# Kernel optimization log

Hardware: AMD Instinct MI355X
Metric: run time of the kernel (lower is better)

## Reference

```python
import jax, jax.numpy as jnp
import numpy as np

B, T, D, R = 4, 2048, 1024, 64

def setup_inputs() -> dict:
    key = jax.random.key(0)
    ks = jax.random.split(key, 13)
    x = jax.random.normal(ks[0], (B, T, D), jnp.float32)
    # Linear weights stored torch-style [out, in]; applied as x @ W.T
    WQ = jax.random.normal(ks[1], (D, D), jnp.float32) * 0.02
    WK = jax.random.normal(ks[2], (D, D), jnp.float32) * 0.02
    WO = jax.random.normal(ks[3], (D, D), jnp.float32) * 0.02
    Winv = jnp.eye(D, dtype=jnp.float32) + 0.01 * jax.random.normal(ks[4], (D, D), jnp.float32)
    U_b = jax.random.normal(ks[5], (D, R), jnp.float32) * 0.02
    V_b = jax.random.normal(ks[6], (D, R), jnp.float32) * 0.02
    W_b = jax.random.normal(ks[7], (D, R), jnp.float32) * 0.02
    bias_b = jnp.zeros((D,), jnp.float32)
    U_t = jax.random.normal(ks[8], (D, R), jnp.float32) * 0.02
    V_t = jax.random.normal(ks[9], (D, R), jnp.float32) * 0.02
    W_t = jax.random.normal(ks[10], (D, R), jnp.float32) * 0.02
    X_t = jax.random.normal(ks[11], (D, R), jnp.float32) * 0.02
    bias_t = jnp.zeros((D,), jnp.float32)
    alpha_bi = jnp.float32(0.5)
    alpha_tri = jnp.float32(0.5)
    return {"x": x, "WQ": WQ, "WK": WK, "WO": WO, "Winv": Winv,
            "U_b": U_b, "V_b": V_b, "W_b": W_b, "bias_b": bias_b,
            "U_t": U_t, "V_t": V_t, "W_t": W_t, "X_t": X_t, "bias_t": bias_t,
            "alpha_bi": alpha_bi, "alpha_tri": alpha_tri}


def reference(x, WQ, WK, WO, Winv, U_b, V_b, W_b, bias_b,
              U_t, V_t, W_t, X_t, bias_t, alpha_bi, alpha_tri):
    # Faithful forward. The original materializes [B,T,T,D] pairwise tensors,
    # masks causally, sums over j and divides by n_valid. Because the (i,j)
    # score factorizes as f(i)*g(j) in rank space, sum_{j<=i} == f(i)*cumsum(g)_i,
    # so we use causal cumulative sums -- identical math, O(B*T*D*R) memory.
    Tlen = x.shape[1]
    Q = x @ WQ.T                       # [B,T,D]
    K = x @ WK.T
    invQ = Q @ Winv.T
    invK = K @ Winv.T
    counts = jnp.arange(1, Tlen + 1, dtype=x.dtype)[None, :, None]  # [1,T,1]
    z = jnp.cumsum(x, axis=1) / counts  # causal global mean, [B,T,D]
    # bilinear forward: sum_{j<=i} ((Q_i V_b) * (K_j W_b)) U_b^T + bias_b
    fwd_r = (Q @ V_b) * jnp.cumsum(K @ W_b, axis=1)          # [B,T,R]
    # bilinear inverse: sum_{j<=i} ((invK_j V_b) * (invQ_i W_b)) U_b^T + bias_b
    inv_r = jnp.cumsum(invK @ V_b, axis=1) * (invQ @ W_b)    # [B,T,R]
    # trilinear: sum_{j<=i} ((Q_i V_t)*(K_j W_t)*(Z_i X_t)) U_t^T + bias_t
    tri_r = (Q @ V_t) * jnp.cumsum(K @ W_t, axis=1) * (z @ X_t)  # [B,T,R]
    sum_fwd = fwd_r @ U_b.T + counts * bias_b                # [B,T,D]
    sum_inv = inv_r @ U_b.T + counts * bias_b
    sum_tri = tri_r @ U_t.T + counts * bias_t
    out = (sum_fwd + alpha_bi * sum_inv + alpha_tri * sum_tri) / counts
    return out @ WO.T
```

## Files before the change

kernel.cpp:

```cpp
#include <hip/hip_runtime.h>

#define T_LEN 2048
#define BT_DIM 8192

typedef __attribute__((ext_vector_type(8))) short s16x8;
typedef __attribute__((ext_vector_type(4))) float f32x4;

typedef __attribute__((address_space(1))) void gvoid_t;
typedef __attribute__((address_space(3))) void svoid_t;

__device__ __forceinline__ unsigned short f2bf(float f) {
  unsigned int u = __builtin_bit_cast(unsigned int, f);
  u += 0x7fffu + ((u >> 16) & 1u);
  return (unsigned short)(u >> 16);
}
__device__ __forceinline__ float bf2f(unsigned short u) {
  unsigned int v = (unsigned int)u << 16;
  return __builtin_bit_cast(float, v);
}
__device__ __forceinline__ void gload16(const void* g, void* l) {
  __builtin_amdgcn_global_load_lds((gvoid_t*)g, (svoid_t*)l, 16, 0, 0);
}

template<int EPI>
__device__ __forceinline__ void gemm_body(
    const unsigned short* __restrict__ A, const unsigned short* __restrict__ B,
    void* __restrict__ Cv, int lda, int ldb, int ldc, int K, int m0, int n0,
    const float* __restrict__ obias, float* __restrict__ sums, int ygrp,
    int rlo, int rhi)
{
  __shared__ unsigned short As[2 * 128 * 64];
  __shared__ unsigned short Bs[2 * 128 * 64];
  const int tid  = threadIdx.x;
  const int wave = tid >> 6;
  const int lane = tid & 63;
  const int wr = wave >> 1, wc = wave & 1;
  const int trow = tid >> 3;
  const int tcol = (tid & 7) << 3;

  const unsigned short* Ap = A + (size_t)(m0 + trow) * lda + tcol;
  const unsigned short* Bp = B + (size_t)(n0 + trow) * ldb + tcol;

  f32x4 acc[4][4] = {};

  auto stage = [&](int buf, int kt) {
    char* ab = (char*)As + buf * 16384 + wave * 1024;
    char* bb = (char*)Bs + buf * 16384 + wave * 1024;
#pragma unroll
    for (int it = 0; it < 4; ++it) {
      gload16(Ap + (size_t)it * 32 * lda + kt, ab + it * 4096);
      gload16(Bp + (size_t)it * 32 * ldb + kt, bb + it * 4096);
    }
  };

  stage(0, 0);
  __syncthreads();
  int cur = 0;
  for (int kt = 64; kt <= K; kt += 64) {
    if (kt < K) stage(cur ^ 1, kt);
#pragma unroll
    for (int ks = 0; ks < 2; ++ks) {
      const int kk = (ks << 5) + ((lane >> 4) << 3);
      const int ra = (wr << 6) + (lane & 15);
      const int rb = (wc << 6) + (lane & 15);
      s16x8 af[4], bfr[4];
#pragma unroll
      for (int i = 0; i < 4; ++i)
        af[i] = *(const s16x8*)&As[cur * 8192 + (ra + (i << 4)) * 64 + kk];
#pragma unroll
      for (int i = 0; i < 4; ++i)
        bfr[i] = *(const s16x8*)&Bs[cur * 8192 + (rb + (i << 4)) * 64 + kk];
#pragma unroll
      for (int i = 0; i < 4; ++i)
#pragma unroll
        for (int j = 0; j < 4; ++j)
          acc[i][j] = __builtin_amdgcn_mfma_f32_16x16x32_bf16(af[i], bfr[j], acc[i][j], 0, 0, 0);
    }
    __syncthreads();
    cur ^= 1;
  }

  if (EPI == 2) {
    unsigned short* C = (unsigned short*)Cv;
#pragma unroll
    for (int i = 0; i < 4; ++i) {
      const int lr0 = (wr << 6) + (i << 4) + ((lane >> 4) << 2);
#pragma unroll
      for (int j = 0; j < 4; ++j) {
        const int c = n0 + (wc << 6) + (j << 4) + (lane & 15);
#pragma unroll
        for (int rr = 0; rr < 4; ++rr) {
          const int lr = lr0 + rr;
          if (lr >= rlo && lr < rhi)
            C[(size_t)(m0 + lr) * ldc + c] = f2bf(acc[i][j][rr]);
        }
      }
    }
  } else if (EPI == 3) {
    float* C = (float*)Cv;
    float ob[4];
#pragma unroll
    for (int j = 0; j < 4; ++j)
      ob[j] = obias[n0 + (wc << 6) + (j << 4) + (lane & 15)];
#pragma unroll
    for (int i = 0; i < 4; ++i) {
      const int r0 = m0 + (wr << 6) + (i << 4) + ((lane >> 4) << 2);
#pragma unroll
      for (int j = 0; j < 4; ++j) {
        const int c = n0 + (wc << 6) + (j << 4) + (lane & 15);
#pragma unroll
        for (int rr = 0; rr < 4; ++rr)
          C[(size_t)(r0 + rr) * ldc + c] = acc[i][j][rr] + ob[j];
      }
    }
  } else {
    unsigned short* C = (unsigned short*)Cv;
#pragma unroll
    for (int i = 0; i < 4; ++i) {
      const int r0 = m0 + (wr << 6) + (i << 4) + ((lane >> 4) << 2);
#pragma unroll
      for (int j = 0; j < 4; ++j) {
        const int c = (wc << 6) + (j << 4) + (lane & 15);
#pragma unroll
        for (int rr = 0; rr < 4; ++rr)
          C[(size_t)(r0 + rr) * ldc + c] = f2bf(acc[i][j][rr]);
      }
    }
    int soff = -1;
    if (ygrp == 1) soff = wc << 6;
    else if (ygrp == 2 && wc == 0) soff = 128;
    else if (ygrp == 3 && wc == 0) soff = 192;
    if (soff >= 0) {
#pragma unroll
      for (int half = 0; half < 2; ++half) {
        const int grow = m0 + (wr << 6) + (half << 5);
        const int b_ = grow >> 11, ch = (grow & 2047) >> 5;
#pragma unroll
        for (int j = 0; j < 4; ++j) {
          float v = 0.f;
#pragma unroll
          for (int i = half * 2; i < half * 2 + 2; ++i)
#pragma unroll
            for (int rr = 0; rr < 4; ++rr) v += acc[i][j][rr];
          v += __shfl_xor(v, 16);
          v += __shfl_xor(v, 32);
          if (lane < 16)
            sums[((b_ * 64 + ch) << 8) + soff + (j << 4) + lane] = v;
        }
      }
    }
  }
}

__global__ __launch_bounds__(256) void smallA_k(
    const unsigned short* BQ, const unsigned short* BK, const unsigned short* BI,
    const unsigned short* WOb, const unsigned short* WQt, const unsigned short* WKt,
    const unsigned short* Winvt, const unsigned short* UcatT,
    unsigned short* Gcat, unsigned short* Hb, unsigned short* Gfin)
{
  const int bx = blockIdx.x;
  const unsigned short *A, *B; unsigned short* C; int ldc, m0, n0;
  switch (blockIdx.y) {
    case 0:  A = BQ;  B = WQt;   C = Gcat;              ldc = 1024; m0 = 0; n0 = bx * 128; break;
    case 1:  A = BK;  B = WKt;   C = Gcat + 128 * 1024; ldc = 1024; m0 = 0; n0 = bx * 128; break;
    case 2:  A = BI;  B = Winvt; C = Hb;                ldc = 1024; m0 = 0; n0 = bx * 128; break;
    default: A = WOb; B = UcatT; C = Gfin;              ldc = 128;  m0 = bx * 128; n0 = 0; break;
  }
  gemm_body<2>(A, B, C, 1024, 1024, ldc, 1024, m0, n0, nullptr, nullptr, 0, 0, 128);
}

__global__ __launch_bounds__(256) void smallB_k(
    const unsigned short* Hb, const unsigned short* WKt, const unsigned short* WQt,
    unsigned short* Gcat)
{
  const int bx = blockIdx.x;
  const unsigned short* B = (blockIdx.y == 0) ? WKt : WQt;
  const int rlo = (blockIdx.y == 0) ? 0 : 64;
  gemm_body<2>(Hb, B, Gcat + 256 * 1024, 1024, 1024, 1024, 1024, 0, bx * 128,
               nullptr, nullptr, 0, rlo, rlo + 64);
}

__global__ __launch_bounds__(256) void mainP_k(
    const unsigned short* __restrict__ xb, const unsigned short* __restrict__ Gcat,
    unsigned short* __restrict__ Pcat, float* __restrict__ sums)
{
  const int y = blockIdx.y;
  gemm_body<4>(xb, Gcat + (size_t)y * 128 * 1024, Pcat + y * 128,
               1024, 1024, 512, 1024, blockIdx.x * 128, 0, nullptr, sums, y, 0, 128);
}

__global__ __launch_bounds__(256) void final_k(
    const unsigned short* __restrict__ rcat, const unsigned short* __restrict__ Gfin,
    const float* __restrict__ obias, float* __restrict__ out)
{
  gemm_body<3>(rcat, Gfin, out, 128, 128, 1024, 128,
               blockIdx.x * 128, blockIdx.y * 128, obias, nullptr, 0, 0, 128);
}

__global__ __launch_bounds__(256) void prep_k(
    const float* __restrict__ x, const float* __restrict__ WQ,
    const float* __restrict__ WK, const float* __restrict__ WO,
    const float* __restrict__ Winv, const float* __restrict__ U_b,
    const float* __restrict__ V_b, const float* __restrict__ W_b,
    const float* __restrict__ bias_b, const float* __restrict__ U_t,
    const float* __restrict__ V_t, const float* __restrict__ W_t,
    const float* __restrict__ X_t, const float* __restrict__ bias_t,
    const float* __restrict__ abi_p, const float* __restrict__ atri_p,
    unsigned short* xb, unsigned short* WQt, unsigned short* WKt,
    unsigned short* Winvt, unsigned short* WOb, unsigned short* BQ,
    unsigned short* BK, unsigned short* BI, unsigned short* UcatT,
    unsigned short* Gcat, float* obias)
{
  __shared__ float smem[64 * 65];
  const int bx = blockIdx.x, tid = threadIdx.x;
  if (bx < 8192) {
    int i = bx * 256 + tid;
    float4 v = ((const float4*)x)[i];
    ushort4 o; o.x = f2bf(v.x); o.y = f2bf(v.y); o.z = f2bf(v.z); o.w = f2bf(v.w);
    ((ushort4*)xb)[i] = o;
  } else if (bx < 8960) {
    int local = bx - 8192;
    const float* s; unsigned short* d;
    switch (local >> 8) { case 0: s = WQ; d = WQt; break;
                          case 1: s = WK; d = WKt; break;
                          default: s = Winv; d = Winvt; break; }
    int t = local & 255;
    int tY = t >> 4, tX = t & 15;
    int c = tid & 63, g = tid >> 6;
#pragma unroll
    for (int rr = 0; rr < 16; ++rr) {
      int r = g * 16 + rr;
      smem[r * 65 + c] = s[(size_t)(tY * 64 + r) * 1024 + tX * 64 + c];
    }
    __syncthreads();
#pragma unroll
    for (int rr = 0; rr < 16; ++rr) {
      int r = g * 16 + rr;
      d[(size_t)(tX * 64 + r) * 1024 + tY * 64 + c] = f2bf(smem[c * 65 + r]);
    }
  } else if (bx < 10496) {
    int local = bx - 8960;
    const float *s0, *s1; unsigned short* d;
    switch (local >> 9) { case 0: s0 = V_b; s1 = V_t; d = BQ; break;
                          case 1: s0 = W_b; s1 = W_t; d = BK; break;
                          default: s0 = V_b; s1 = W_b; d = BI; break; }
    int idx = (local & 511) * 256 + tid;
    int n = idx >> 10, k = idx & 1023;
    const float* s = (n < 64) ? s0 : s1;
    d[idx] = f2bf(s[k * 64 + (n & 63)]);
  } else if (bx < 11008) {
    int idx = (bx - 10496) * 256 + tid;
    int k = idx >> 10, dd = idx & 1023;
    UcatT[idx] = f2bf(k < 64 ? U_b[dd * 64 + k] : U_t[dd * 64 + k - 64]);
  } else if (bx < 11520) {
    int idx = (bx - 11008) * 256 + tid;
    int r = idx >> 10, dd = idx & 1023;
    Gcat[(size_t)384 * 1024 + idx] = f2bf(X_t[dd * 64 + (r & 63)]);
  } else if (bx < 12544) {
    int i = (bx - 11520) * 256 + tid;
    float4 v = ((const float4*)WO)[i];
    ushort4 o; o.x = f2bf(v.x); o.y = f2bf(v.y); o.z = f2bf(v.z); o.w = f2bf(v.w);
    ((ushort4*)WOb)[i] = o;
  } else {
    int n = bx - 12544;
    const float abi = abi_p[0], atri = atri_p[0];
    float s = 0.f;
    for (int d0 = tid; d0 < 1024; d0 += 256)
      s += ((1.f + abi) * bias_b[d0] + atri * bias_t[d0]) * WO[(size_t)n * 1024 + d0];
    smem[tid] = s;
    __syncthreads();
#pragma unroll
    for (int w = 128; w > 0; w >>= 1) {
      if (tid < w) smem[tid] += smem[tid + w];
      __syncthreads();
    }
    if (tid == 0) obias[n] = smem[0];
  }
}

__global__ __launch_bounds__(256) void scanB_k(
    const unsigned short* __restrict__ P, const float* __restrict__ sums,
    const float* __restrict__ abi_p, const float* __restrict__ atri_p,
    unsigned short* __restrict__ rcat)
{
  const int w = blockIdx.x * 4 + (threadIdx.x >> 6);
  const int lane = threadIdx.x & 63;
  const int b = w >> 6, ch = w & 63;
  float c2 = 0.f, c6 = 0.f, c3 = 0.f, cZ = 0.f;
  for (int i = 0; i < ch; ++i) {
    const float* s = sums + (((size_t)b * 64 + i) << 8) + lane;
    c2 += s[0]; c6 += s[64]; c3 += s[128]; cZ += s[192];
  }
  const float abi = abi_p[0], atri = atri_p[0];
  const size_t row0 = (size_t)b * T_LEN + ch * 32;
#pragma unroll 2
  for (int t = 0; t < 32; ++t) {
    const size_t ro = (row0 + t) * 512;
    const float p1 = bf2f(P[ro + lane]);
    const float p5 = bf2f(P[ro + 64 + lane]);
    c2 += bf2f(P[ro + 128 + lane]);
    c6 += bf2f(P[ro + 192 + lane]);
    c3 += bf2f(P[ro + 256 + lane]);
    const float p4 = bf2f(P[ro + 320 + lane]);
    cZ += bf2f(P[ro + 384 + lane]);
    const float invc = 1.0f / (float)(ch * 32 + t + 1);
    const float rb = (p1 * c2 + abi * (c3 * p4)) * invc;
    const float rt = atri * p5 * c6 * cZ * invc * invc;
    const size_t rro = (row0 + t) * 128;
    rcat[rro + lane]      = f2bf(rb);
    rcat[rro + 64 + lane] = f2bf(rt);
  }
}

extern "C" void kernel_launch(void* const* d_in, const int* in_sizes, int n_in,
                              void* d_out, int out_size, void* d_ws, size_t ws_size,
                              hipStream_t stream)
{
  const float* x      = (const float*)d_in[0];
  const float* WQ     = (const float*)d_in[1];
  const float* WK     = (const float*)d_in[2];
  const float* WO     = (const float*)d_in[3];
  const float* Winv   = (const float*)d_in[4];
  const float* U_b    = (const float*)d_in[5];
  const float* V_b    = (const float*)d_in[6];
  const float* W_b    = (const float*)d_in[7];
  const float* bias_b = (const float*)d_in[8];
  const float* U_t    = (const float*)d_in[9];
  const float* V_t    = (const float*)d_in[10];
  const float* W_t    = (const float*)d_in[11];
  const float* X_t    = (const float*)d_in[12];
  const float* bias_t = (const float*)d_in[13];
  const float* a_bi   = (const float*)d_in[14];
  const float* a_tri  = (const float*)d_in[15];

  char* ws = (char*)d_ws;
  size_t off = 0;
  unsigned short* xb    = (unsigned short*)(ws + off); off += (size_t)BT_DIM * 1024 * 2;
  unsigned short* Pcat  = (unsigned short*)(ws + off); off += (size_t)BT_DIM * 512 * 2;
  unsigned short* rcat  = (unsigned short*)(ws + off); off += (size_t)BT_DIM * 128 * 2;
  unsigned short* WQt   = (unsigned short*)(ws + off); off += 2097152;
  unsigned short* WKt   = (unsigned short*)(ws + off); off += 2097152;
  unsigned short* Winvt = (unsigned short*)(ws + off); off += 2097152;
  unsigned short* WOb   = (unsigned short*)(ws + off); off += 2097152;
  unsigned short* BQ    = (unsigned short*)(ws + off); off += 262144;
  unsigned short* BK    = (unsigned short*)(ws + off); off += 262144;
  unsigned short* BI    = (unsigned short*)(ws + off); off += 262144;
  unsigned short* Hb    = (unsigned short*)(ws + off); off += 262144;
  unsigned short* UcatT = (unsigned short*)(ws + off); off += 262144;
  unsigned short* Gcat  = (unsigned short*)(ws + off); off += (size_t)512 * 1024 * 2;
  unsigned short* Gfin  = (unsigned short*)(ws + off); off += 262144;
  float*          obias = (float*)(ws + off);          off += 4096;
  float*          sums  = (float*)(ws + off);          off += 262144;

  prep_k<<<dim3(13568), 256, 0, stream>>>(x, WQ, WK, WO, Winv, U_b, V_b, W_b, bias_b,
                                          U_t, V_t, W_t, X_t, bias_t, a_bi, a_tri,
                                          xb, WQt, WKt, Winvt, WOb, BQ, BK, BI,
                                          UcatT, Gcat, obias);
  smallA_k<<<dim3(8, 4), 256, 0, stream>>>(BQ, BK, BI, WOb, WQt, WKt, Winvt, UcatT,
                                           Gcat, Hb, Gfin);
  smallB_k<<<dim3(8, 2), 256, 0, stream>>>(Hb, WKt, WQt, Gcat);
  mainP_k<<<dim3(64, 4), 256, 0, stream>>>(xb, Gcat, Pcat, sums);
  scanB_k<<<dim3(64), 256, 0, stream>>>(Pcat, sums, a_bi, a_tri, rcat);
  final_k<<<dim3(64, 8), 256, 0, stream>>>(rcat, Gfin, obias, (float*)d_out);
}
```

Measured before the change: 210.1 us.

## Split-K main GEMM in two, XOR-swizzle LDS, finer scan chunks

```diff
diff --git a/kernel.cpp b/kernel.cpp
--- a/kernel.cpp
+++ b/kernel.cpp
@@ -36,10 +36,10 @@
   const int lane = tid & 63;
   const int wr = wave >> 1, wc = wave & 1;
   const int trow = tid >> 3;
-  const int tcol = (tid & 7) << 3;
-
-  const unsigned short* Ap = A + (size_t)(m0 + trow) * lda + tcol;
-  const unsigned short* Bp = B + (size_t)(n0 + trow) * ldb + tcol;
+  const int scol = (((tid & 7) ^ ((tid >> 3) & 7)) << 3);
+
+  const unsigned short* Ap = A + (size_t)(m0 + trow) * lda + scol;
+  const unsigned short* Bp = B + (size_t)(n0 + trow) * ldb + scol;
 
   f32x4 acc[4][4] = {};
 
@@ -56,11 +56,12 @@
   stage(0, 0);
   __syncthreads();
   int cur = 0;
+  const int xr = (lane & 7) << 3;
   for (int kt = 64; kt <= K; kt += 64) {
     if (kt < K) stage(cur ^ 1, kt);
 #pragma unroll
     for (int ks = 0; ks < 2; ++ks) {
-      const int kk = (ks << 5) + ((lane >> 4) << 3);
+      const int kk = ((ks << 5) + ((lane >> 4) << 3)) ^ xr;
       const int ra = (wr << 6) + (lane & 15);
       const int rb = (wc << 6) + (lane & 15);
       s16x8 af[4], bfr[4];
@@ -132,20 +133,16 @@
     else if (ygrp == 3 && wc == 0) soff = 192;
     if (soff >= 0) {
 #pragma unroll
-      for (int half = 0; half < 2; ++half) {
-        const int grow = m0 + (wr << 6) + (half << 5);
-        const int b_ = grow >> 11, ch = (grow & 2047) >> 5;
+      for (int i = 0; i < 4; ++i) {
+        const int R0 = m0 + (wr << 6) + (i << 4);
+        const int b_ = R0 >> 11, ch = (R0 & 2047) >> 4;
 #pragma unroll
         for (int j = 0; j < 4; ++j) {
-          float v = 0.f;
-#pragma unroll
-          for (int i = half * 2; i < half * 2 + 2; ++i)
-#pragma unroll
-            for (int rr = 0; rr < 4; ++rr) v += acc[i][j][rr];
+          float v = acc[i][j][0] + acc[i][j][1] + acc[i][j][2] + acc[i][j][3];
           v += __shfl_xor(v, 16);
           v += __shfl_xor(v, 32);
           if (lane < 16)
-            sums[((b_ * 64 + ch) << 8) + soff + (j << 4) + lane] = v;
+            sums[(((b_ << 7) + ch) << 8) + soff + (j << 4) + lane] = v;
         }
       }
     }
@@ -184,9 +181,11 @@
     const unsigned short* __restrict__ xb, const unsigned short* __restrict__ Gcat,
     unsigned short* __restrict__ Pcat, float* __restrict__ sums)
 {
-  const int y = blockIdx.y;
-  gemm_body<4>(xb, Gcat + (size_t)y * 128 * 1024, Pcat + y * 128,
-               1024, 1024, 512, 1024, blockIdx.x * 128, 0, nullptr, sums, y, 0, 128);
+  const int y = blockIdx.y, kz = blockIdx.z;
+  gemm_body<4>(xb + kz * 512, Gcat + (size_t)y * 128 * 1024 + kz * 512,
+               Pcat + (size_t)kz * BT_DIM * 512 + y * 128,
+               1024, 1024, 512, 512, blockIdx.x * 128, 0,
+               nullptr, sums + kz * 131072, y, 0, 128);
 }
 
 __global__ __launch_bounds__(256) void final_k(
@@ -285,25 +284,30 @@
 {
   const int w = blockIdx.x * 4 + (threadIdx.x >> 6);
   const int lane = threadIdx.x & 63;
-  const int b = w >> 6, ch = w & 63;
+  const int b = w >> 7, ch = w & 127;
   float c2 = 0.f, c6 = 0.f, c3 = 0.f, cZ = 0.f;
   for (int i = 0; i < ch; ++i) {
-    const float* s = sums + (((size_t)b * 64 + i) << 8) + lane;
-    c2 += s[0]; c6 += s[64]; c3 += s[128]; cZ += s[192];
+    const float* s0 = sums + ((((size_t)b << 7) + i) << 8) + lane;
+    const float* s1 = s0 + 131072;
+    c2 += s0[0]   + s1[0];
+    c6 += s0[64]  + s1[64];
+    c3 += s0[128] + s1[128];
+    cZ += s0[192] + s1[192];
   }
   const float abi = abi_p[0], atri = atri_p[0];
-  const size_t row0 = (size_t)b * T_LEN + ch * 32;
+  const size_t row0 = (size_t)b * T_LEN + ch * 16;
+  const unsigned short* P1 = P + (size_t)BT_DIM * 512;
 #pragma unroll 2
-  for (int t = 0; t < 32; ++t) {
-    const size_t ro = (row0 + t) * 512;
-    const float p1 = bf2f(P[ro + lane]);
-    const float p5 = bf2f(P[ro + 64 + lane]);
-    c2 += bf2f(P[ro + 128 + lane]);
-    c6 += bf2f(P[ro + 192 + lane]);
-    c3 += bf2f(P[ro + 256 + lane]);
-    const float p4 = bf2f(P[ro + 320 + lane]);
-    cZ += bf2f(P[ro + 384 + lane]);
-    const float invc = 1.0f / (float)(ch * 32 + t + 1);
+  for (int t = 0; t < 16; ++t) {
+    const size_t ro = (row0 + t) * 512 + lane;
+    const float p1 = bf2f(P[ro])       + bf2f(P1[ro]);
+    const float p5 = bf2f(P[ro + 64])  + bf2f(P1[ro + 64]);
+    c2            += bf2f(P[ro + 128]) + bf2f(P1[ro + 128]);
+    c6            += bf2f(P[ro + 192]) + bf2f(P1[ro + 192]);
+    c3            += bf2f(P[ro + 256]) + bf2f(P1[ro + 256]);
+    const float p4 = bf2f(P[ro + 320]) + bf2f(P1[ro + 320]);
+    cZ            += bf2f(P[ro + 384]) + bf2f(P1[ro + 384]);
+    const float invc = 1.0f / (float)(ch * 16 + t + 1);
     const float rb = (p1 * c2 + abi * (c3 * p4)) * invc;
     const float rt = atri * p5 * c6 * cZ * invc * invc;
     const size_t rro = (row0 + t) * 128;
@@ -336,7 +340,7 @@
   char* ws = (char*)d_ws;
   size_t off = 0;
   unsigned short* xb    = (unsigned short*)(ws + off); off += (size_t)BT_DIM * 1024 * 2;
-  unsigned short* Pcat  = (unsigned short*)(ws + off); off += (size_t)BT_DIM * 512 * 2;
+  unsigned short* Pcat  = (unsigned short*)(ws + off); off += (size_t)2 * BT_DIM * 512 * 2;
   unsigned short* rcat  = (unsigned short*)(ws + off); off += (size_t)BT_DIM * 128 * 2;
   unsigned short* WQt   = (unsigned short*)(ws + off); off += 2097152;
   unsigned short* WKt   = (unsigned short*)(ws + off); off += 2097152;
@@ -350,7 +354,7 @@
   unsigned short* Gcat  = (unsigned short*)(ws + off); off += (size_t)512 * 1024 * 2;
   unsigned short* Gfin  = (unsigned short*)(ws + off); off += 262144;
   float*          obias = (float*)(ws + off);          off += 4096;
-  float*          sums  = (float*)(ws + off);          off += 262144;
+  float*          sums  = (float*)(ws + off);          off += 1048576;
 
   prep_k<<<dim3(13568), 256, 0, stream>>>(x, WQ, WK, WO, Winv, U_b, V_b, W_b, bias_b,
                                           U_t, V_t, W_t, X_t, bias_t, a_bi, a_tri,
@@ -359,7 +363,7 @@
   smallA_k<<<dim3(8, 4), 256, 0, stream>>>(BQ, BK, BI, WOb, WQt, WKt, Winvt, UcatT,
                                            Gcat, Hb, Gfin);
   smallB_k<<<dim3(8, 2), 256, 0, stream>>>(Hb, WKt, WQt, Gcat);
-  mainP_k<<<dim3(64, 4), 256, 0, stream>>>(xb, Gcat, Pcat, sums);
-  scanB_k<<<dim3(64), 256, 0, stream>>>(Pcat, sums, a_bi, a_tri, rcat);
+  mainP_k<<<dim3(64, 4, 2), 256, 0, stream>>>(xb, Gcat, Pcat, sums);
+  scanB_k<<<dim3(128), 256, 0, stream>>>(Pcat, sums, a_bi, a_tri, rcat);
   final_k<<<dim3(64, 8), 256, 0, stream>>>(rcat, Gfin, obias, (float*)d_out);
 }
```

Measured after the change: 219.1 us. 4.3% more time.
